# Kernel optimization log

Measured on AMD Instinct MI355X. Metric: run time of the kernel, lower is better.

Reference implementation:

```python
import jax, jax.numpy as jnp
import numpy as np

D_MODEL = 1024
N_HEADS = 16
HEAD_DIM = D_MODEL // N_HEADS
B, T = 2, 2048


def _rotate_half(x):
    # Faithful to module's _apply_rotary: view (..., D//2, 2), pair -> (-x1, x0)
    xr = x.reshape(*x.shape[:-1], HEAD_DIM // 2, 2)
    rot = jnp.stack([-xr[..., 1], xr[..., 0]], axis=-1)
    return rot.reshape(*x.shape)


def setup_inputs() -> dict:
    key = jax.random.key(0)
    ks = jax.random.split(key, 9)
    s = 1.0 / np.sqrt(D_MODEL)
    return {
        "x": jax.random.normal(ks[0], (B, T, D_MODEL), jnp.float32),
        "Wq": jax.random.normal(ks[1], (D_MODEL, D_MODEL), jnp.float32) * s,
        "bq": jax.random.normal(ks[2], (D_MODEL,), jnp.float32) * 0.02,
        "Wk": jax.random.normal(ks[3], (D_MODEL, D_MODEL), jnp.float32) * s,
        "bk": jax.random.normal(ks[4], (D_MODEL,), jnp.float32) * 0.02,
        "Wv": jax.random.normal(ks[5], (D_MODEL, D_MODEL), jnp.float32) * s,
        "bv": jax.random.normal(ks[6], (D_MODEL,), jnp.float32) * 0.02,
        "Wo": jax.random.normal(ks[7], (D_MODEL, D_MODEL), jnp.float32) * s,
        "bo": jax.random.normal(ks[8], (D_MODEL,), jnp.float32) * 0.02,
    }


def reference(x, Wq, bq, Wk, bk, Wv, bv, Wo, bo):
    b, t, _ = x.shape
    # QKV projections (nn.Linear: x @ W.T + b), split heads -> (B, H, T, Dh)
    def proj(W, bias):
        y = x @ W.T + bias
        return y.reshape(b, t, N_HEADS, HEAD_DIM).transpose(0, 2, 1, 3)

    q = _rotate_half(proj(Wq, bq))
    k = _rotate_half(proj(Wk, bk))
    v = proj(Wv, bv)

    scale = 1.0 / jnp.sqrt(jnp.asarray(HEAD_DIM, x.dtype))
    scores = jnp.einsum('bhqd,bhkd->bhqk', q, k) * scale
    causal = jnp.tril(jnp.ones((t, t), bool))  # (T, T)
    scores = jnp.where(causal, scores, jnp.asarray(-jnp.inf, scores.dtype))
    attn = jax.nn.softmax(scores, axis=-1)
    out = jnp.einsum('bhqk,bhkd->bhqd', attn, v)
    out = out.transpose(0, 2, 1, 3).reshape(b, t, D_MODEL)
    return out @ Wo.T + bo
```

## Files before the change

### kernel.cpp

```cpp
#include <hip/hip_runtime.h>
#include <stdint.h>

#define DM 1024
#define NH 16
#define HD 64
#define BB 2
#define TT 2048
#define MT (BB*TT)

typedef __bf16 bfrag __attribute__((ext_vector_type(8)));
typedef float  f32x4 __attribute__((ext_vector_type(4)));

__device__ __forceinline__ unsigned short f2bf(float f) {
  union { float f; unsigned u; } v; v.f = f;
  unsigned r = v.u + 0x7fffu + ((v.u >> 16) & 1u);
  return (unsigned short)(r >> 16);
}

__device__ __forceinline__ unsigned short f2bf_hw(float f) {
  __bf16 b = (__bf16)f;
  union { __bf16 b; unsigned short u; } v; v.b = b;
  return v.u;
}

__device__ __forceinline__ unsigned int pack2bf(float a, float b) {
  union { __bf16 h[2]; unsigned int u; } v;
  v.h[0] = (__bf16)a; v.h[1] = (__bf16)b;
  return v.u;
}

__device__ __forceinline__ void async16(const void* g, void* l) {
  __builtin_amdgcn_global_load_lds(
      (const __attribute__((address_space(1))) unsigned int*)g,
      (__attribute__((address_space(3))) unsigned int*)l, 16, 0, 0);
}

__global__ __launch_bounds__(256) void cvt_kernel(
    const float* __restrict__ x,  const float* __restrict__ Wq,
    const float* __restrict__ Wk, const float* __restrict__ Wv,
    const float* __restrict__ Wo,
    unsigned short* __restrict__ xb, unsigned short* __restrict__ wqkv,
    unsigned short* __restrict__ wob) {
  int i = blockIdx.x * 256 + threadIdx.x;
  const int NX = MT * DM / 4;
  const int NW = DM * DM / 4;
  const float* src; unsigned short* dst; int off;
  if      (i < NX)        { src = x;  dst = xb;              off = i; }
  else if (i < NX + NW)   { src = Wq; dst = wqkv;            off = i - NX; }
  else if (i < NX + 2*NW) { src = Wk; dst = wqkv + DM*DM;    off = i - NX - NW; }
  else if (i < NX + 3*NW) { src = Wv; dst = wqkv + 2*DM*DM;  off = i - NX - 2*NW; }
  else                    { src = Wo; dst = wob;             off = i - NX - 3*NW; }
  float4 v = ((const float4*)src)[off];
  ushort4 o;
  o.x = f2bf(v.x); o.y = f2bf(v.y); o.z = f2bf(v.z); o.w = f2bf(v.w);
  ((ushort4*)dst)[off] = o;
}

template<int EPI, int TM>
__global__ __launch_bounds__(256) void gemm_bt(
    const unsigned short* __restrict__ A, const unsigned short* __restrict__ Bm,
    const float* __restrict__ bias0, const float* __restrict__ bias1,
    const float* __restrict__ bias2,
    unsigned short* __restrict__ Qo, unsigned short* __restrict__ Ko,
    unsigned short* __restrict__ Vo, float* __restrict__ Co) {
  constexpr int WM = TM / 2;
  constexpr int MI = WM / 16;
  const int tid = threadIdx.x;
  const int wave = tid >> 6, lane = tid & 63;
  const int lr = lane & 15, quad = lane >> 4;
  const int m0 = blockIdx.y * TM, n0 = blockIdx.x * 128;
  __shared__ __align__(16) unsigned short sA[2][TM * 32];
  __shared__ __align__(16) unsigned short sB[2][128 * 32];
  const f32x4 zero = {0.f, 0.f, 0.f, 0.f};
  f32x4 acc[MI][4];
#pragma unroll
  for (int i = 0; i < MI; i++)
#pragma unroll
    for (int j = 0; j < 4; j++) acc[i][j] = zero;
  const int wm = (wave >> 1) * WM, wn = (wave & 1) * 64;

  auto stage = [&](int kt, int buf) {
    const int k0 = kt * 32;
#pragma unroll
    for (int rep = 0; rep < TM / 64; ++rep) {
      int fb = rep * 2048 + wave * 512;
      int fl = fb + lane * 8;
      int row = fl >> 5;
      int c   = (fl >> 3) & 3;
      int col = ((c ^ ((row >> 1) & 3)) << 3);
      async16(A + (size_t)(m0 + row) * 1024 + k0 + col, &sA[buf][fb]);
    }
#pragma unroll
    for (int rep = 0; rep < 2; ++rep) {
      int fb = rep * 2048 + wave * 512;
      int fl = fb + lane * 8;
      int row = fl >> 5;
      int c   = (fl >> 3) & 3;
      int col = ((c ^ ((row >> 1) & 3)) << 3);
      async16(Bm + (size_t)(n0 + row) * 1024 + k0 + col, &sB[buf][fb]);
    }
  };

  stage(0, 0);
  for (int kt = 0; kt < 32; ++kt) {
    const int buf = kt & 1;
    __syncthreads();
    if (kt + 1 < 32) stage(kt + 1, buf ^ 1);
    bfrag af[MI], bfr[4];
#pragma unroll
    for (int i = 0; i < MI; i++) {
      int ra = wm + i * 16 + lr;
      af[i]  = *(const bfrag*)&sA[buf][ra * 32 + ((quad ^ ((ra >> 1) & 3)) << 3)];
    }
#pragma unroll
    for (int j = 0; j < 4; j++) {
      int rb = wn + j * 16 + lr;
      bfr[j] = *(const bfrag*)&sB[buf][rb * 32 + ((quad ^ ((rb >> 1) & 3)) << 3)];
    }
#pragma unroll
    for (int i = 0; i < MI; i++)
#pragma unroll
      for (int j = 0; j < 4; j++)
        acc[i][j] = __builtin_amdgcn_mfma_f32_16x16x32_bf16(af[i], bfr[j], acc[i][j], 0, 0, 0);
  }

  if (EPI == 0) {
#pragma unroll
    for (int j = 0; j < 4; j++) {
      int n = n0 + wn + j * 16 + lr;
      int qkv = n >> 10, nn = n & 1023;
      float bias = (qkv == 0 ? bias0 : qkv == 1 ? bias1 : bias2)[nn];
      int h = nn >> 6, d = nn & 63;
      if (qkv == 2) {
#pragma unroll
        for (int i = 0; i < MI; i++) {
          int t0 = m0 + wm + i * 16 + quad * 4;
          int b = t0 >> 11, tt = t0 & 2047;
          size_t bb = (size_t)((b << 4) + h) * (TT * 64);
          int kk0 = tt & 63;
          size_t off = bb + (size_t)(tt >> 6) * 4096 +
                       (size_t)((kk0 >> 3) << 9) + (d << 3) + (kk0 & 7);
          ushort4 pk;
          pk.x = f2bf(acc[i][j][0] + bias);
          pk.y = f2bf(acc[i][j][1] + bias);
          pk.z = f2bf(acc[i][j][2] + bias);
          pk.w = f2bf(acc[i][j][3] + bias);
          *(ushort4*)(Vo + off) = pk;
        }
      } else {
#pragma unroll
        for (int i = 0; i < MI; i++)
#pragma unroll
          for (int r = 0; r < 4; r++) {
            int m = m0 + wm + i * 16 + quad * 4 + r;
            float vb = acc[i][j][r] + bias;
            float pv = __shfl_xor(vb, 1);
            float val = (n & 1) ? pv : -pv;
            int b = m >> 11, t = m & 2047;
            size_t base = (size_t)((b << 4) + h) * (TT * 64);
            if (qkv == 0) {
              Qo[base + (size_t)t * 64 + d] = f2bf(val * 0.125f);
            } else {
              int kk = t & 63;
              size_t off = base + (size_t)(t >> 6) * 4096 +
                           (size_t)((d >> 3) << 9) + (kk << 3) + (d & 7);
              Ko[off] = f2bf(val);
            }
          }
      }
    }
  } else {
#pragma unroll
    for (int j = 0; j < 4; j++) {
      int n = n0 + wn + j * 16 + lr;
      float bias = bias0[n];
#pragma unroll
      for (int i = 0; i < MI; i++)
#pragma unroll
        for (int r = 0; r < 4; r++) {
          int m = m0 + wm + i * 16 + quad * 4 + r;
          Co[(size_t)m * 1024 + n] = acc[i][j][r] + bias;
        }
    }
  }
}

__global__ __launch_bounds__(256) void gemm_op(
    const unsigned short* __restrict__ A, const unsigned short* __restrict__ Bm,
    const float* __restrict__ bias0, float* __restrict__ Co) {
  const int tid = threadIdx.x;
  const int wave = tid >> 6, lane = tid & 63;
  const int lr = lane & 15, quad = lane >> 4;
  const int m0 = blockIdx.y * 64, n0 = blockIdx.x * 128;
  __shared__ __align__(16) unsigned short sA[2][64 * 64];
  __shared__ __align__(16) unsigned short sB[2][128 * 64];
  const f32x4 zero = {0.f, 0.f, 0.f, 0.f};
  f32x4 acc[2][4];
#pragma unroll
  for (int i = 0; i < 2; i++)
#pragma unroll
    for (int j = 0; j < 4; j++) acc[i][j] = zero;
  const int wm = (wave >> 1) * 32, wn = (wave & 1) * 64;

  auto swz = [](int row) { return ((row & 1) << 2) | ((row >> 1) & 3); };

  auto stage = [&](int kt, int buf) {
    const int k0 = kt * 64;
#pragma unroll
    for (int rep = 0; rep < 2; ++rep) {
      int fb = rep * 2048 + wave * 512;
      int fl = fb + lane * 8;
      int row = fl >> 6, pc = (fl >> 3) & 7;
      async16(A + (size_t)(m0 + row) * 1024 + k0 + ((pc ^ swz(row)) << 3), &sA[buf][fb]);
    }
#pragma unroll
    for (int rep = 0; rep < 4; ++rep) {
      int fb = rep * 2048 + wave * 512;
      int fl = fb + lane * 8;
      int row = fl >> 6, pc = (fl >> 3) & 7;
      async16(Bm + (size_t)(n0 + row) * 1024 + k0 + ((pc ^ swz(row)) << 3), &sB[buf][fb]);
    }
  };

  stage(0, 0);
  for (int kt = 0; kt < 16; ++kt) {
    const int buf = kt & 1;
    __syncthreads();
    if (kt + 1 < 16) stage(kt + 1, buf ^ 1);
#pragma unroll
    for (int ks = 0; ks < 2; ++ks) {
      bfrag af[2], bfr[4];
#pragma unroll
      for (int i = 0; i < 2; i++) {
        int ra = wm + i * 16 + lr;
        af[i] = *(const bfrag*)&sA[buf][ra * 64 + (((ks * 4 + quad) ^ swz(ra)) << 3)];
      }
#pragma unroll
      for (int j = 0; j < 4; j++) {
        int rb = wn + j * 16 + lr;
        bfr[j] = *(const bfrag*)&sB[buf][rb * 64 + (((ks * 4 + quad) ^ swz(rb)) << 3)];
      }
#pragma unroll
      for (int i = 0; i < 2; i++)
#pragma unroll
        for (int j = 0; j < 4; j++)
          acc[i][j] = __builtin_amdgcn_mfma_f32_16x16x32_bf16(af[i], bfr[j], acc[i][j], 0, 0, 0);
    }
  }

#pragma unroll
  for (int j = 0; j < 4; j++) {
    int n = n0 + wn + j * 16 + lr;
    float bias = bias0[n];
#pragma unroll
    for (int i = 0; i < 2; i++)
#pragma unroll
      for (int r = 0; r < 4; r++) {
        int m = m0 + wm + i * 16 + quad * 4 + r;
        Co[(size_t)m * 1024 + n] = acc[i][j][r] + bias;
      }
  }
}

__global__ __launch_bounds__(512, 4) void flash_kernel(
    const unsigned short* __restrict__ Qg, const unsigned short* __restrict__ Kg,
    const unsigned short* __restrict__ Vg, unsigned short* __restrict__ Og) {
  const int p = blockIdx.x;
  const int bh = blockIdx.y;
  const int tid = threadIdx.x, wave = tid >> 6, lane = tid & 63;
  const int lr = lane & 15, quad = lane >> 4;
  __shared__ __align__(16) unsigned short sK[2][8192];
  __shared__ __align__(16) unsigned short sV[2][8192];
  __shared__ __align__(16) unsigned short sP[8][1024];
  const size_t base = (size_t)bh * (TT * 64);
  const int st = wave >> 2;
  const int qt = st ? p : (31 - p);
  const int nS = st ? (p + 1) : (32 - p);
  const int nB = 32 - p;
  const int npair = (nB + 1) >> 1;
  const int qg = qt * 64 + (wave & 3) * 16 + lr;
  const f32x4 zero = {0.f, 0.f, 0.f, 0.f};

  bfrag qf0, qf1;
  {
    const unsigned short* qr = Qg + base + (size_t)qg * 64;
    qf0 = *(const bfrag*)(qr + quad * 8);
    qf1 = *(const bfrag*)(qr + 32 + quad * 8);
  }
  f32x4 o[4];
  float rs = 0.f;
#pragma unroll
  for (int j = 0; j < 4; j++) o[j] = zero;

  const unsigned short* kgb = Kg + base;
  const unsigned short* vgb = Vg + base;

#pragma unroll
  for (int rep = 0; rep < 2; ++rep) {
    int fb = rep * 4096 + wave * 512;
    async16(kgb + fb + lane * 8, &sK[0][fb]);
    async16(vgb + fb + lane * 8, &sV[0][fb]);
  }

  const int pwr = lr * 8 + (quad & 1) * 4;
  const int pq2 = quad >> 1;

  for (int ktb = 0; ktb < npair; ++ktb) {
    const int buf = ktb & 1;
    __syncthreads();
    if (ktb + 1 < npair) {
#pragma unroll
      for (int rep = 0; rep < 2; ++rep) {
        int fb = rep * 4096 + wave * 512;
        const size_t g = (size_t)(ktb + 1) * 8192 + fb + lane * 8;
        async16(kgb + g, &sK[buf ^ 1][fb]);
        async16(vgb + g, &sV[buf ^ 1][fb]);
      }
    }
#pragma unroll
    for (int sub = 0; sub < 2; ++sub) {
      const int kt = ktb * 2 + sub;
      if (kt < nS) {
        const int hb = sub * 4096;
        f32x4 sT[4];
#pragma unroll
        for (int ct = 0; ct < 4; ct++) {
          int row8 = (ct * 16 + lr) * 8;
          bfrag k0 = *(const bfrag*)&sK[buf][hb + quad * 512 + row8];
          bfrag k1 = *(const bfrag*)&sK[buf][hb + (4 + quad) * 512 + row8];
          f32x4 t = __builtin_amdgcn_mfma_f32_16x16x32_bf16(k0, qf0, zero, 0, 0, 0);
          sT[ct]  = __builtin_amdgcn_mfma_f32_16x16x32_bf16(k1, qf1, t,    0, 0, 0);
        }
        const bool diag = (kt == nS - 1);
#pragma unroll
        for (int ct = 0; ct < 4; ++ct) {
          float e[4];
#pragma unroll
          for (int r = 0; r < 4; ++r)
            e[r] = __expf(sT[ct][r] - 11.0f);
          if (diag) {
#pragma unroll
            for (int r = 0; r < 4; ++r) {
              int key = kt * 64 + ct * 16 + quad * 4 + r;
              if (key > qg) e[r] = 0.f;
            }
          }
          rs += (e[0] + e[1]) + (e[2] + e[3]);
          uint2 w;
          w.x = pack2bf(e[0], e[1]);
          w.y = pack2bf(e[2], e[3]);
          *(uint2*)&sP[wave][(ct * 2 + pq2) * 128 + pwr] = w;
        }
        bfrag pf0 = *(const bfrag*)&sP[wave][quad * 128 + lr * 8];
        bfrag pf1 = *(const bfrag*)&sP[wave][(4 + quad) * 128 + lr * 8];
#pragma unroll
        for (int j = 0; j < 4; j++) {
          int row8 = (j * 16 + lr) * 8;
          bfrag v0 = *(const bfrag*)&sV[buf][hb + quad * 512 + row8];
          bfrag v1 = *(const bfrag*)&sV[buf][hb + (4 + quad) * 512 + row8];
          o[j] = __builtin_amdgcn_mfma_f32_16x16x32_bf16(v0, pf0, o[j], 0, 0, 0);
          o[j] = __builtin_amdgcn_mfma_f32_16x16x32_bf16(v1, pf1, o[j], 0, 0, 0);
        }
      }
    }
  }

  rs += __shfl_xor(rs, 16); rs += __shfl_xor(rs, 32);
  const float inv = 1.0f / rs;

  const int b = bh >> 4, h = bh & 15;
#pragma unroll
  for (int j = 0; j < 4; j++) {
    ushort4 pk;
    pk.x = f2bf_hw(o[j][0] * inv); pk.y = f2bf_hw(o[j][1] * inv);
    pk.z = f2bf_hw(o[j][2] * inv); pk.w = f2bf_hw(o[j][3] * inv);
    int col = h * 64 + j * 16 + quad * 4;
    *(ushort4*)(Og + (size_t)(b * TT + qg) * 1024 + col) = pk;
  }
}

extern "C" void kernel_launch(void* const* d_in, const int* in_sizes, int n_in,
                              void* d_out, int out_size, void* d_ws, size_t ws_size,
                              hipStream_t stream) {
  const float* x  = (const float*)d_in[0];
  const float* Wq = (const float*)d_in[1];
  const float* bq = (const float*)d_in[2];
  const float* Wk = (const float*)d_in[3];
  const float* bk = (const float*)d_in[4];
  const float* Wv = (const float*)d_in[5];
  const float* bv = (const float*)d_in[6];
  const float* Wo = (const float*)d_in[7];
  const float* bo = (const float*)d_in[8];
  float* out = (float*)d_out;

  unsigned short* ws = (unsigned short*)d_ws;
  unsigned short* xb   = ws;
  unsigned short* wqkv = ws + (size_t)4 * 1024 * 1024;
  unsigned short* wob  = ws + (size_t)7 * 1024 * 1024;
  unsigned short* Qb   = ws + (size_t)8 * 1024 * 1024;
  unsigned short* Kb   = ws + (size_t)12 * 1024 * 1024;
  unsigned short* Vb   = ws + (size_t)16 * 1024 * 1024;
  unsigned short* Ob   = ws + (size_t)20 * 1024 * 1024;

  cvt_kernel<<<dim3(8192), dim3(256), 0, stream>>>(x, Wq, Wk, Wv, Wo, xb, wqkv, wob);
  gemm_bt<0, 128><<<dim3(24, 32), dim3(256), 0, stream>>>(xb, wqkv, bq, bk, bv,
                                                          Qb, Kb, Vb, (float*)nullptr);
  flash_kernel<<<dim3(16, 32), dim3(512), 0, stream>>>(Qb, Kb, Vb, Ob);
  gemm_op<<<dim3(8, 64), dim3(256), 0, stream>>>(Ob, wob, bo, out);
}
```

Measured before the change: 187.2 us.

## Rewrite QKV GEMM with 256x256 tiles, 8 waves, and fine-grained async pipeline

Replaces the templated 128x128-tile QKV projection GEMM with a dedicated kernel that uses 256x256 output tiles, 512 threads (8 waves), and a 64-wide K step split into two 32-wide halves. Global-to-LDS async loads are issued in small parts interleaved between MFMA phases, with explicit vmcnt waits, raw barriers and s_setprio around the MFMA blocks. A swizzled block index remaps the 192 tiles so that blocks running together share input tiles in cache. The goal is more data reuse per LDS load and better overlap of memory with matrix math. In exchange it uses more LDS (128KB) and more registers per block, which lowers occupancy, and it relies on hand-tuned wait counts that are easy to get wrong.

```diff
diff --git a/kernel.cpp b/kernel.cpp
--- a/kernel.cpp
+++ b/kernel.cpp
@@ -34,6 +34,10 @@
       (const __attribute__((address_space(1))) unsigned int*)g,
       (__attribute__((address_space(3))) unsigned int*)l, 16, 0, 0);
 }
+
+#define CBAR() do { asm volatile("" ::: "memory"); \
+                    __builtin_amdgcn_s_barrier();  \
+                    asm volatile("" ::: "memory"); } while (0)
 
 __global__ __launch_bounds__(256) void cvt_kernel(
     const float* __restrict__ x,  const float* __restrict__ Wq,
@@ -56,130 +60,153 @@
   ((ushort4*)dst)[off] = o;
 }
 
-template<int EPI, int TM>
-__global__ __launch_bounds__(256) void gemm_bt(
+__global__ __launch_bounds__(512, 2) void gemm_qkv(
     const unsigned short* __restrict__ A, const unsigned short* __restrict__ Bm,
     const float* __restrict__ bias0, const float* __restrict__ bias1,
     const float* __restrict__ bias2,
     unsigned short* __restrict__ Qo, unsigned short* __restrict__ Ko,
-    unsigned short* __restrict__ Vo, float* __restrict__ Co) {
-  constexpr int WM = TM / 2;
-  constexpr int MI = WM / 16;
+    unsigned short* __restrict__ Vo) {
   const int tid = threadIdx.x;
   const int wave = tid >> 6, lane = tid & 63;
   const int lr = lane & 15, quad = lane >> 4;
-  const int m0 = blockIdx.y * TM, n0 = blockIdx.x * 128;
-  __shared__ __align__(16) unsigned short sA[2][TM * 32];
-  __shared__ __align__(16) unsigned short sB[2][128 * 32];
+  const int flat = blockIdx.x;
+  const int s = (flat & 7) * 24 + (flat >> 3);
+  const int m0 = (s / 12) * 256, n0 = (s % 12) * 256;
+
+  __shared__ __align__(16) unsigned short sA[2][2][256 * 32];
+  __shared__ __align__(16) unsigned short sB[2][2][256 * 32];
+
   const f32x4 zero = {0.f, 0.f, 0.f, 0.f};
-  f32x4 acc[MI][4];
-#pragma unroll
-  for (int i = 0; i < MI; i++)
+  f32x4 acc[8][4];
+#pragma unroll
+  for (int i = 0; i < 8; i++)
 #pragma unroll
     for (int j = 0; j < 4; j++) acc[i][j] = zero;
-  const int wm = (wave >> 1) * WM, wn = (wave & 1) * 64;
-
-  auto stage = [&](int kt, int buf) {
-    const int k0 = kt * 32;
-#pragma unroll
-    for (int rep = 0; rep < TM / 64; ++rep) {
-      int fb = rep * 2048 + wave * 512;
+
+  const int wm = (wave >> 2) * 128, wn = (wave & 3) * 64;
+
+  auto stagePart = [&](int h) {
+    if (h >= 64) return;
+    const int ts = h >> 2, pi = h & 3;
+    const int buf = ts & 1, hk = pi >> 1;
+    const unsigned short* src = (pi & 1) ? Bm : A;
+    const int r0 = (pi & 1) ? n0 : m0;
+    unsigned short* dst = (pi & 1) ? &sB[buf][hk][0] : &sA[buf][hk][0];
+    const int k0 = ts * 64 + (hk << 5);
+#pragma unroll
+    for (int rep = 0; rep < 2; ++rep) {
+      int fb = rep * 4096 + wave * 512;
       int fl = fb + lane * 8;
       int row = fl >> 5;
       int c   = (fl >> 3) & 3;
-      int col = ((c ^ ((row >> 1) & 3)) << 3);
-      async16(A + (size_t)(m0 + row) * 1024 + k0 + col, &sA[buf][fb]);
-    }
-#pragma unroll
-    for (int rep = 0; rep < 2; ++rep) {
-      int fb = rep * 2048 + wave * 512;
-      int fl = fb + lane * 8;
-      int row = fl >> 5;
-      int c   = (fl >> 3) & 3;
-      int col = ((c ^ ((row >> 1) & 3)) << 3);
-      async16(Bm + (size_t)(n0 + row) * 1024 + k0 + col, &sB[buf][fb]);
+      async16(src + (size_t)(r0 + row) * 1024 + k0 + ((c ^ ((row >> 1) & 3)) << 3),
+              dst + fb);
     }
   };
 
-  stage(0, 0);
-  for (int kt = 0; kt < 32; ++kt) {
-    const int buf = kt & 1;
-    __syncthreads();
-    if (kt + 1 < 32) stage(kt + 1, buf ^ 1);
-    bfrag af[MI], bfr[4];
-#pragma unroll
-    for (int i = 0; i < MI; i++) {
-      int ra = wm + i * 16 + lr;
-      af[i]  = *(const bfrag*)&sA[buf][ra * 32 + ((quad ^ ((ra >> 1) & 3)) << 3)];
-    }
-#pragma unroll
-    for (int j = 0; j < 4; j++) {
-      int rb = wn + j * 16 + lr;
-      bfr[j] = *(const bfrag*)&sB[buf][rb * 32 + ((quad ^ ((rb >> 1) & 3)) << 3)];
-    }
-#pragma unroll
-    for (int i = 0; i < MI; i++)
-#pragma unroll
-      for (int j = 0; j < 4; j++)
-        acc[i][j] = __builtin_amdgcn_mfma_f32_16x16x32_bf16(af[i], bfr[j], acc[i][j], 0, 0, 0);
-  }
-
-  if (EPI == 0) {
-#pragma unroll
-    for (int j = 0; j < 4; j++) {
-      int n = n0 + wn + j * 16 + lr;
-      int qkv = n >> 10, nn = n & 1023;
-      float bias = (qkv == 0 ? bias0 : qkv == 1 ? bias1 : bias2)[nn];
-      int h = nn >> 6, d = nn & 63;
-      if (qkv == 2) {
-#pragma unroll
-        for (int i = 0; i < MI; i++) {
-          int t0 = m0 + wm + i * 16 + quad * 4;
-          int b = t0 >> 11, tt = t0 & 2047;
-          size_t bb = (size_t)((b << 4) + h) * (TT * 64);
-          int kk0 = tt & 63;
-          size_t off = bb + (size_t)(tt >> 6) * 4096 +
-                       (size_t)((kk0 >> 3) << 9) + (d << 3) + (kk0 & 7);
-          ushort4 pk;
-          pk.x = f2bf(acc[i][j][0] + bias);
-          pk.y = f2bf(acc[i][j][1] + bias);
-          pk.z = f2bf(acc[i][j][2] + bias);
-          pk.w = f2bf(acc[i][j][3] + bias);
-          *(ushort4*)(Vo + off) = pk;
-        }
-      } else {
-#pragma unroll
-        for (int i = 0; i < MI; i++)
-#pragma unroll
-          for (int r = 0; r < 4; r++) {
-            int m = m0 + wm + i * 16 + quad * 4 + r;
-            float vb = acc[i][j][r] + bias;
-            float pv = __shfl_xor(vb, 1);
-            float val = (n & 1) ? pv : -pv;
-            int b = m >> 11, t = m & 2047;
-            size_t base = (size_t)((b << 4) + h) * (TT * 64);
-            if (qkv == 0) {
-              Qo[base + (size_t)t * 64 + d] = f2bf(val * 0.125f);
-            } else {
-              int kk = t & 63;
-              size_t off = base + (size_t)(t >> 6) * 4096 +
-                           (size_t)((d >> 3) << 9) + (kk << 3) + (d & 7);
-              Ko[off] = f2bf(val);
-            }
-          }
-      }
-    }
-  } else {
-#pragma unroll
-    for (int j = 0; j < 4; j++) {
-      int n = n0 + wn + j * 16 + lr;
-      float bias = bias0[n];
-#pragma unroll
-      for (int i = 0; i < MI; i++)
+#pragma unroll
+  for (int h = 0; h < 6; ++h) stagePart(h);
+  asm volatile("s_waitcnt vmcnt(8)" ::: "memory");
+  CBAR();
+
+  bfrag af[4], bf[4];
+#pragma unroll 1
+  for (int t = 0; t < 16; ++t) {
+    const int buf = t & 1;
+    const int P0 = 4 * t;
+
+    auto rdA = [&](int hk, int ihalf) {
+#pragma unroll
+      for (int i = 0; i < 4; i++) {
+        int ra = wm + ihalf * 64 + i * 16 + lr;
+        af[i] = *(const bfrag*)&sA[buf][hk][ra * 32 + ((quad ^ ((ra >> 1) & 3)) << 3)];
+      }
+    };
+    auto rdB = [&](int hk) {
+#pragma unroll
+      for (int j = 0; j < 4; j++) {
+        int rb = wn + j * 16 + lr;
+        bf[j] = *(const bfrag*)&sB[buf][hk][rb * 32 + ((quad ^ ((rb >> 1) & 3)) << 3)];
+      }
+    };
+    auto domfma = [&](int ib) {
+      __builtin_amdgcn_s_setprio(1);
+#pragma unroll
+      for (int i = 0; i < 4; i++)
+#pragma unroll
+        for (int j = 0; j < 4; j++)
+          acc[ib + i][j] = __builtin_amdgcn_mfma_f32_16x16x32_bf16(
+              af[i], bf[j], acc[ib + i][j], 0, 0, 0);
+      __builtin_amdgcn_s_setprio(0);
+    };
+
+    rdA(0, 0); rdB(0);
+    stagePart(P0 + 6);
+    CBAR();
+    domfma(0);
+    CBAR();
+    rdA(0, 1);
+    stagePart(P0 + 7);
+    if (t == 15) { asm volatile("s_waitcnt vmcnt(0)" ::: "memory"); }
+    else         { asm volatile("s_waitcnt vmcnt(8)" ::: "memory"); }
+    CBAR();
+    domfma(4);
+    CBAR();
+    rdA(1, 0); rdB(1);
+    stagePart(P0 + 8);
+    CBAR();
+    domfma(0);
+    CBAR();
+    rdA(1, 1);
+    stagePart(P0 + 9);
+    if (t == 14)      { asm volatile("s_waitcnt vmcnt(4)" ::: "memory"); }
+    else if (t < 14)  { asm volatile("s_waitcnt vmcnt(8)" ::: "memory"); }
+    CBAR();
+    domfma(4);
+    CBAR();
+  }
+
+#pragma unroll
+  for (int j = 0; j < 4; j++) {
+    int n = n0 + wn + j * 16 + lr;
+    int qkv = n >> 10, nn = n & 1023;
+    float bias = (qkv == 0 ? bias0 : qkv == 1 ? bias1 : bias2)[nn];
+    int h = nn >> 6, d = nn & 63;
+    if (qkv == 2) {
+#pragma unroll
+      for (int i = 0; i < 8; i++) {
+        int t0 = m0 + wm + i * 16 + quad * 4;
+        int b = t0 >> 11, tt = t0 & 2047;
+        size_t bb = (size_t)((b << 4) + h) * (TT * 64);
+        int kk0 = tt & 63;
+        size_t off = bb + (size_t)(tt >> 6) * 4096 +
+                     (size_t)((kk0 >> 3) << 9) + (d << 3) + (kk0 & 7);
+        ushort4 pk;
+        pk.x = f2bf(acc[i][j][0] + bias);
+        pk.y = f2bf(acc[i][j][1] + bias);
+        pk.z = f2bf(acc[i][j][2] + bias);
+        pk.w = f2bf(acc[i][j][3] + bias);
+        *(ushort4*)(Vo + off) = pk;
+      }
+    } else {
+#pragma unroll
+      for (int i = 0; i < 8; i++)
 #pragma unroll
         for (int r = 0; r < 4; r++) {
           int m = m0 + wm + i * 16 + quad * 4 + r;
-          Co[(size_t)m * 1024 + n] = acc[i][j][r] + bias;
+          float vb = acc[i][j][r] + bias;
+          float pv = __shfl_xor(vb, 1);
+          float val = (n & 1) ? pv : -pv;
+          int b = m >> 11, t = m & 2047;
+          size_t base = (size_t)((b << 4) + h) * (TT * 64);
+          if (qkv == 0) {
+            Qo[base + (size_t)t * 64 + d] = f2bf(val * 0.125f);
+          } else {
+            int kk = t & 63;
+            size_t off = base + (size_t)(t >> 6) * 4096 +
+                         (size_t)((d >> 3) << 9) + (kk << 3) + (d & 7);
+            Ko[off] = f2bf(val);
+          }
         }
     }
   }
@@ -403,8 +430,7 @@
   unsigned short* Ob   = ws + (size_t)20 * 1024 * 1024;
 
   cvt_kernel<<<dim3(8192), dim3(256), 0, stream>>>(x, Wq, Wk, Wv, Wo, xb, wqkv, wob);
-  gemm_bt<0, 128><<<dim3(24, 32), dim3(256), 0, stream>>>(xb, wqkv, bq, bk, bv,
-                                                          Qb, Kb, Vb, (float*)nullptr);
+  gemm_qkv<<<dim3(192), dim3(512), 0, stream>>>(xb, wqkv, bq, bk, bv, Qb, Kb, Vb);
   flash_kernel<<<dim3(16, 32), dim3(512), 0, stream>>>(Qb, Kb, Vb, Ob);
   gemm_op<<<dim3(8, 64), dim3(256), 0, stream>>>(Ob, wob, bo, out);
 }
```

New measurement: 188.3 us. About the same (+0.6%).
